# Kernel optimization log

Hardware: AMD Instinct MI355X
Metric: run time of the kernel (lower is better)

Reference implementation:

```python
import jax, jax.numpy as jnp
import numpy as np

B, T = 16384, 64
VOCAB, EMB, HID = 1001, 16, 1024


def setup_inputs() -> dict:
    key = jax.random.key(0)
    k1, k2, k3, k4, k5, k6 = jax.random.split(key, 6)
    xis = jax.random.randint(k1, (B, T), 0, VOCAB, dtype=jnp.int32)
    emb = jax.random.normal(k2, (VOCAB, EMB), dtype=jnp.float32)
    lif_w = jax.random.normal(k3, (EMB, HID), dtype=jnp.float32) / np.sqrt(EMB)
    lif_b = jax.random.normal(k4, (HID,), dtype=jnp.float32) * 0.01
    fc_w = jax.random.normal(k5, (HID, 1), dtype=jnp.float32) / np.sqrt(HID)
    fc_b = jax.random.normal(k6, (1,), dtype=jnp.float32) * 0.01
    alpha = jnp.float32(0.3)   # LIF membrane decay (soma_params='all_share' scalar)
    beta = jnp.float32(0.0)    # LIF additive bias
    return {"xis": xis, "emb": emb, "lif_w": lif_w, "lif_b": lif_b,
            "fc_w": fc_w, "fc_b": fc_b, "alpha": alpha, "beta": beta}


def reference(xis, emb, lif_w, lif_b, fc_w, fc_b, alpha, beta):
    # Per-timestep: embedding lookup -> FcLif (linear + LIF membrane recurrence,
    # analog mode) -> dropout (eval: identity) -> fc. Only the last timestep's
    # fc output is returned by the original loop; only v carries across steps.
    x_emb = emb[xis]                     # [B, T, EMB]
    x_tbd = jnp.swapaxes(x_emb, 0, 1)    # [T, B, EMB] for scan over time

    def step(v, x_t):
        x1 = x_t @ lif_w + lif_b         # [B, HID] synaptic current
        v = alpha * v + x1 + beta        # membrane update (reset(x1) -> v0 = 0)
        return v, None

    v0 = jnp.zeros((B, HID), dtype=x_emb.dtype)
    vT, _ = jax.lax.scan(step, v0, x_tbd)
    o = jax.nn.relu(vT)                  # analog (cmode='analog') soma output
    out = (o @ fc_w + fc_b)[:, 0]        # [B]
    return out
```

## Files before the change

kernel.cpp:

```cpp
#include <hip/hip_runtime.h>
#include <hip/hip_bf16.h>


#define BB    16384
#define TT    64
#define EMBD  16
#define HIDD  1024
#define ROWS  32
#define NTHR  512
#define NBLK  (BB / ROWS)
#define XWPAD 24
#define HTPW  8

typedef __attribute__((ext_vector_type(8))) short          frag_ab;
typedef __attribute__((ext_vector_type(4))) float          frag_cd;
typedef __attribute__((ext_vector_type(4))) unsigned short us4;

__device__ __forceinline__ unsigned short f2b(float f) {
    __hip_bfloat16 h = __float2bfloat16(f);
    return __builtin_bit_cast(unsigned short, h);
}

__global__ __launch_bounds__(NTHR, 4)
void ftt_kernel(const int* __restrict__ xis, const float* __restrict__ emb,
                const float* __restrict__ lif_w, const float* __restrict__ lif_b,
                const float* __restrict__ fc_w, const float* __restrict__ fc_b,
                const float* __restrict__ alpha_p, const float* __restrict__ beta_p,
                float* __restrict__ out)
{
    __shared__ unsigned short xwb[ROWS * XWPAD];
    __shared__ float red[ROWS / 16][8][16];

    const int tid  = threadIdx.x;
    const int lane = tid & 63;
    const int wave = tid >> 6;
    const int row0 = blockIdx.x * ROWS;
    const float alpha = alpha_p[0];
    const float beta  = beta_p[0];

    const float a2  = alpha * alpha;
    const float a4  = a2 * a2;
    const float a8  = a4 * a4;
    const float a16 = a8 * a8;
    const float a32 = a16 * a16;
    const float a48 = a32 * a16;
    const float a64 = a32 * a32;
    const float S   = (fabsf(1.f - alpha) < 1e-8f) ? (float)TT
                                                   : (1.f - a64) / (1.f - alpha);

    const int nn = lane & 15;
    const int kg = lane >> 4;

    frag_ab bfrag[HTPW];
    float   biasr[HTPW], fcwr[HTPW];
    #pragma unroll
    for (int j = 0; j < HTPW; ++j) {
        const int h = wave * (HTPW * 16) + j * 16 + nn;
        biasr[j] = S * (lif_b[h] + beta);
        fcwr[j]  = fc_w[h];
        frag_ab b = {0, 0, 0, 0, 0, 0, 0, 0};
        if (kg < 2) {
            #pragma unroll
            for (int i = 0; i < 8; ++i)
                b[i] = (short)f2b(lif_w[(kg * 8 + i) * HIDD + h]);
        }
        bfrag[j] = b;
    }

    {
        const int r   = tid >> 4;
        const int sub = tid & 15;
        const int c   = sub >> 2;
        const int q   = sub & 3;
        const int4* xp = (const int4*)(xis + (size_t)(row0 + r) * TT + c * 16);
        const float* eb = emb + q * 4;
        float ax = 0.f, ay = 0.f, az = 0.f, aw = 0.f;
        float w = 1.f;
        #pragma unroll
        for (int cc = 3; cc >= 0; --cc) {
            const int4 iv = xp[cc];
            { const float4 e = *(const float4*)(eb + ((size_t)iv.w << 4));
              ax += w * e.x; ay += w * e.y; az += w * e.z; aw += w * e.w; w *= alpha; }
            { const float4 e = *(const float4*)(eb + ((size_t)iv.z << 4));
              ax += w * e.x; ay += w * e.y; az += w * e.z; aw += w * e.w; w *= alpha; }
            { const float4 e = *(const float4*)(eb + ((size_t)iv.y << 4));
              ax += w * e.x; ay += w * e.y; az += w * e.z; aw += w * e.w; w *= alpha; }
            { const float4 e = *(const float4*)(eb + ((size_t)iv.x << 4));
              ax += w * e.x; ay += w * e.y; az += w * e.z; aw += w * e.w; w *= alpha; }
        }
        const float sc = (c == 3) ? 1.f : ((c == 2) ? a16 : ((c == 1) ? a32 : a48));
        ax *= sc; ay *= sc; az *= sc; aw *= sc;
        ax += __shfl_xor(ax, 4); ay += __shfl_xor(ay, 4);
        az += __shfl_xor(az, 4); aw += __shfl_xor(aw, 4);
        ax += __shfl_xor(ax, 8); ay += __shfl_xor(ay, 8);
        az += __shfl_xor(az, 8); aw += __shfl_xor(aw, 8);
        if (c == 0) {
            us4 u = { f2b(ax), f2b(ay), f2b(az), f2b(aw) };
            *(us4*)&xwb[r * XWPAD + q * 4] = u;
        }
    }
    __syncthreads();

    #pragma unroll
    for (int rt = 0; rt < ROWS / 16; ++rt) {
        frag_ab a = {0, 0, 0, 0, 0, 0, 0, 0};
        if (kg < 2)
            a = *(const frag_ab*)&xwb[(rt * 16 + nn) * XWPAD + kg * 8];
        frag_cd pacc = {0.f, 0.f, 0.f, 0.f};
        #pragma unroll
        for (int j = 0; j < HTPW; ++j) {
            frag_cd z = { biasr[j], biasr[j], biasr[j], biasr[j] };
            frag_cd c = __builtin_amdgcn_mfma_f32_16x16x32_bf16(a, bfrag[j], z, 0, 0, 0);
            #pragma unroll
            for (int x = 0; x < 4; ++x)
                pacc[x] += fmaxf(c[x], 0.f) * fcwr[j];
        }
        #pragma unroll
        for (int m = 1; m <= 8; m <<= 1) {
            #pragma unroll
            for (int x = 0; x < 4; ++x) pacc[x] += __shfl_xor(pacc[x], m);
        }
        if (nn == 0) {
            #pragma unroll
            for (int x = 0; x < 4; ++x)
                red[rt][wave][kg * 4 + x] = pacc[x];
        }
    }
    __syncthreads();

    if (tid < ROWS) {
        float s = fc_b[0];
        #pragma unroll
        for (int w2 = 0; w2 < 8; ++w2) s += red[tid >> 4][w2][tid & 15];
        out[row0 + tid] = s;
    }
}

extern "C" void kernel_launch(void* const* d_in, const int* in_sizes, int n_in,
                              void* d_out, int out_size, void* d_ws, size_t ws_size,
                              hipStream_t stream) {
    const int*   xis   = (const int*)d_in[0];
    const float* emb   = (const float*)d_in[1];
    const float* lif_w = (const float*)d_in[2];
    const float* lif_b = (const float*)d_in[3];
    const float* fc_w  = (const float*)d_in[4];
    const float* fc_b  = (const float*)d_in[5];
    const float* alpha = (const float*)d_in[6];
    const float* beta  = (const float*)d_in[7];
    float* out = (float*)d_out;

    ftt_kernel<<<NBLK, NTHR, 0, stream>>>(
        xis, emb, lif_w, lif_b, fc_w, fc_b, alpha, beta, out);
}
```

Measured before the change: 16.18 us.

## Precompute packed bf16 weights and embedding table in a prep kernel

Adds a small prep kernel that packs lif_w into MFMA B-fragment layout as bf16, precomputes the scaled bias and fc weights, and converts the embedding table to bf16 in workspace. The main kernel then loads each fragment with one 16-byte load per lane instead of eight strided scalar loads per block. It also gathers half-width embedding rows. This trades a second launch and a dependency between kernels for less redundant per-block weight conversion and less gather traffic. Rounding the embeddings to bf16 before accumulation adds precision loss.

```diff
diff --git a/kernel.cpp b/kernel.cpp
--- a/kernel.cpp
+++ b/kernel.cpp
@@ -6,37 +6,94 @@
 #define TT    64
 #define EMBD  16
 #define HIDD  1024
+#define NVOC  1001
 #define ROWS  32
 #define NTHR  512
 #define NBLK  (BB / ROWS)
 #define XWPAD 24
 #define HTPW  8
 
+#define WS_WBIAS 65536
+#define WS_WFCW  69632
+#define WS_EMBB  73728
+
 typedef __attribute__((ext_vector_type(8))) short          frag_ab;
 typedef __attribute__((ext_vector_type(4))) float          frag_cd;
 typedef __attribute__((ext_vector_type(4))) unsigned short us4;
 
+__device__ __forceinline__ float bf2f(unsigned short u) {
+    union { unsigned int i; float f; } x; x.i = ((unsigned int)u) << 16; return x.f;
+}
 __device__ __forceinline__ unsigned short f2b(float f) {
     __hip_bfloat16 h = __float2bfloat16(f);
     return __builtin_bit_cast(unsigned short, h);
 }
 
+__global__ __launch_bounds__(256)
+void ftt_prep(const float* __restrict__ emb, const float* __restrict__ lif_w,
+              const float* __restrict__ lif_b, const float* __restrict__ fc_w,
+              const float* __restrict__ alpha_p, const float* __restrict__ beta_p,
+              void* __restrict__ ws)
+{
+    const int s = blockIdx.x * 256 + threadIdx.x;
+    uint4* wpack          = (uint4*)ws;
+    float* wbias          = (float*)((char*)ws + WS_WBIAS);
+    float* wfcw           = (float*)((char*)ws + WS_WFCW);
+    unsigned short* embb  = (unsigned short*)((char*)ws + WS_EMBB);
+
+    if (s < 4096) {
+        const int j2 = s >> 6;
+        const int l  = s & 63;
+        const int kg = l >> 4;
+        const int nn = l & 15;
+        uint4 u = {0u, 0u, 0u, 0u};
+        if (kg < 2) {
+            unsigned int t[8];
+            #pragma unroll
+            for (int i = 0; i < 8; ++i)
+                t[i] = (unsigned int)f2b(lif_w[(kg * 8 + i) * HIDD + j2 * 16 + nn]);
+            u.x = t[0] | (t[1] << 16);
+            u.y = t[2] | (t[3] << 16);
+            u.z = t[4] | (t[5] << 16);
+            u.w = t[6] | (t[7] << 16);
+        }
+        wpack[s] = u;
+    } else if (s < 4096 + 4004) {
+        const int e = s - 4096;
+        const int v = e >> 2, q = e & 3;
+        const float4 f = *(const float4*)(emb + (size_t)v * EMBD + q * 4);
+        us4 u = { f2b(f.x), f2b(f.y), f2b(f.z), f2b(f.w) };
+        *(us4*)&embb[v * EMBD + q * 4] = u;
+    } else if (s >= 8192 && s < 8192 + HIDD) {
+        const int h = s - 8192;
+        const float alpha = alpha_p[0];
+        const float a2 = alpha * alpha, a4 = a2 * a2, a8 = a4 * a4;
+        const float a16 = a8 * a8, a32 = a16 * a16, a64 = a32 * a32;
+        const float S = (fabsf(1.f - alpha) < 1e-8f) ? (float)TT
+                                                     : (1.f - a64) / (1.f - alpha);
+        wbias[h] = S * (lif_b[h] + beta_p[0]);
+        wfcw[h]  = fc_w[h];
+    }
+}
+
 __global__ __launch_bounds__(NTHR, 4)
-void ftt_kernel(const int* __restrict__ xis, const float* __restrict__ emb,
-                const float* __restrict__ lif_w, const float* __restrict__ lif_b,
-                const float* __restrict__ fc_w, const float* __restrict__ fc_b,
-                const float* __restrict__ alpha_p, const float* __restrict__ beta_p,
+void ftt_kernel(const int* __restrict__ xis, const float* __restrict__ fc_b,
+                const float* __restrict__ alpha_p, const void* __restrict__ ws,
                 float* __restrict__ out)
 {
     __shared__ unsigned short xwb[ROWS * XWPAD];
     __shared__ float red[ROWS / 16][8][16];
+
+    const uint4* wpack           = (const uint4*)ws;
+    const float* wbias           = (const float*)((const char*)ws + WS_WBIAS);
+    const float* wfcw            = (const float*)((const char*)ws + WS_WFCW);
+    const unsigned short* embb   = (const unsigned short*)((const char*)ws + WS_EMBB);
 
     const int tid  = threadIdx.x;
     const int lane = tid & 63;
     const int wave = tid >> 6;
     const int row0 = blockIdx.x * ROWS;
     const float alpha = alpha_p[0];
-    const float beta  = beta_p[0];
 
     const float a2  = alpha * alpha;
     const float a4  = a2 * a2;
@@ -44,9 +101,6 @@
     const float a16 = a8 * a8;
     const float a32 = a16 * a16;
     const float a48 = a32 * a16;
-    const float a64 = a32 * a32;
-    const float S   = (fabsf(1.f - alpha) < 1e-8f) ? (float)TT
-                                                   : (1.f - a64) / (1.f - alpha);
 
     const int nn = lane & 15;
     const int kg = lane >> 4;
@@ -55,16 +109,11 @@
     float   biasr[HTPW], fcwr[HTPW];
     #pragma unroll
     for (int j = 0; j < HTPW; ++j) {
-        const int h = wave * (HTPW * 16) + j * 16 + nn;
-        biasr[j] = S * (lif_b[h] + beta);
-        fcwr[j]  = fc_w[h];
-        frag_ab b = {0, 0, 0, 0, 0, 0, 0, 0};
-        if (kg < 2) {
-            #pragma unroll
-            for (int i = 0; i < 8; ++i)
-                b[i] = (short)f2b(lif_w[(kg * 8 + i) * HIDD + h]);
-        }
-        bfrag[j] = b;
+        const int j2 = wave * HTPW + j;
+        bfrag[j] = __builtin_bit_cast(frag_ab, wpack[j2 * 64 + lane]);
+        const int h = j2 * 16 + nn;
+        biasr[j] = wbias[h];
+        fcwr[j]  = wfcw[h];
     }
 
     {
@@ -73,20 +122,24 @@
         const int c   = sub >> 2;
         const int q   = sub & 3;
         const int4* xp = (const int4*)(xis + (size_t)(row0 + r) * TT + c * 16);
-        const float* eb = emb + q * 4;
+        const unsigned short* eb = embb + q * 4;
         float ax = 0.f, ay = 0.f, az = 0.f, aw = 0.f;
         float w = 1.f;
         #pragma unroll
         for (int cc = 3; cc >= 0; --cc) {
             const int4 iv = xp[cc];
-            { const float4 e = *(const float4*)(eb + ((size_t)iv.w << 4));
-              ax += w * e.x; ay += w * e.y; az += w * e.z; aw += w * e.w; w *= alpha; }
-            { const float4 e = *(const float4*)(eb + ((size_t)iv.z << 4));
-              ax += w * e.x; ay += w * e.y; az += w * e.z; aw += w * e.w; w *= alpha; }
-            { const float4 e = *(const float4*)(eb + ((size_t)iv.y << 4));
-              ax += w * e.x; ay += w * e.y; az += w * e.z; aw += w * e.w; w *= alpha; }
-            { const float4 e = *(const float4*)(eb + ((size_t)iv.x << 4));
-              ax += w * e.x; ay += w * e.y; az += w * e.z; aw += w * e.w; w *= alpha; }
+            { const us4 e = *(const us4*)(eb + ((size_t)iv.w << 4));
+              ax += w * bf2f(e.x); ay += w * bf2f(e.y);
+              az += w * bf2f(e.z); aw += w * bf2f(e.w); w *= alpha; }
+            { const us4 e = *(const us4*)(eb + ((size_t)iv.z << 4));
+              ax += w * bf2f(e.x); ay += w * bf2f(e.y);
+              az += w * bf2f(e.z); aw += w * bf2f(e.w); w *= alpha; }
+            { const us4 e = *(const us4*)(eb + ((size_t)iv.y << 4));
+              ax += w * bf2f(e.x); ay += w * bf2f(e.y);
+              az += w * bf2f(e.z); aw += w * bf2f(e.w); w *= alpha; }
+            { const us4 e = *(const us4*)(eb + ((size_t)iv.x << 4));
+              ax += w * bf2f(e.x); ay += w * bf2f(e.y);
+              az += w * bf2f(e.z); aw += w * bf2f(e.w); w *= alpha; }
         }
         const float sc = (c == 3) ? 1.f : ((c == 2) ? a16 : ((c == 1) ? a32 : a48));
         ax *= sc; ay *= sc; az *= sc; aw *= sc;
@@ -149,6 +202,6 @@
     const float* beta  = (const float*)d_in[7];
     float* out = (float*)d_out;
 
-    ftt_kernel<<<NBLK, NTHR, 0, stream>>>(
-        xis, emb, lif_w, lif_b, fc_w, fc_b, alpha, beta, out);
-}
+    ftt_prep<<<36, 256, 0, stream>>>(emb, lif_w, lif_b, fc_w, alpha, beta, d_ws);
+    ftt_kernel<<<NBLK, NTHR, 0, stream>>>(xis, fc_b, alpha, d_ws, out);
+}
```

New measurement: 17.49 us. 8.1% more time.
